# Kernel optimization log

Hardware: AMD Instinct MI355X
Metric: run time of the kernel (lower is better)

Reference implementation:

```python
import jax, jax.numpy as jnp
import numpy as np

B, T, D_MODEL, N_HEADS = 2, 2048, 2048, 16
D_HEAD = D_MODEL // N_HEADS
SCALE = 1.0 / np.sqrt(D_HEAD)


def setup_inputs() -> dict:
    key = jax.random.key(0)
    ks = jax.random.split(key, 5)
    w_std = 1.0 / np.sqrt(D_MODEL)
    x = jax.random.normal(ks[0], (B, T, D_MODEL), dtype=jnp.float32)
    W_q = jax.random.normal(ks[1], (D_MODEL, D_MODEL), dtype=jnp.float32) * w_std
    W_k = jax.random.normal(ks[2], (D_MODEL, D_MODEL), dtype=jnp.float32) * w_std
    W_v = jax.random.normal(ks[3], (D_MODEL, D_MODEL), dtype=jnp.float32) * w_std
    W_o = jax.random.normal(ks[4], (D_MODEL, D_MODEL), dtype=jnp.float32) * w_std
    return {"x": x, "W_q": W_q, "W_k": W_k, "W_v": W_v, "W_o": W_o}


def _split_heads(y):
    # [B, T, D] -> [B, H, T, d_head]
    b, t, _ = y.shape
    return y.reshape(b, t, N_HEADS, D_HEAD).transpose(0, 2, 1, 3)


def reference(x, W_q, W_k, W_v, W_o):
    # Linear layers (torch nn.Linear: y = x @ W.T)
    Q = _split_heads(x @ W_q.T)
    K = _split_heads(x @ W_k.T)
    V = _split_heads(x @ W_v.T)
    # Causal softmax attention (math-equivalent to the tiled online-softmax loop)
    scores = jnp.einsum('bhqd,bhkd->bhqk', Q, K) * SCALE
    causal_mask = jnp.tril(jnp.ones((T, T), dtype=bool))  # [T, T]
    scores = jnp.where(causal_mask, scores, -jnp.inf)
    P = jax.nn.softmax(scores, axis=-1)
    O = jnp.einsum('bhqk,bhkd->bhqd', P, V)
    out = O.transpose(0, 2, 1, 3).reshape(B, T, D_MODEL)  # merge heads
    return out @ W_o.T
```

## Files before the change

kernel.cpp:

```cpp
#include <hip/hip_runtime.h>
#include <hip/hip_bf16.h>
#include <hip/hip_fp16.h>

#define B_   2
#define T_   2048
#define DM   2048
#define NH   16
#define DH   128
#define M_   (B_*T_)
#define SCALE_ 0.08838834764831845f

typedef _Float16 f16;
typedef f16  half8 __attribute__((ext_vector_type(8)));
typedef f16  half4 __attribute__((ext_vector_type(4)));
typedef float f32x4 __attribute__((ext_vector_type(4)));

#define GL16(gp, lp) __builtin_amdgcn_global_load_lds( \
    (const __attribute__((address_space(1))) void*)(gp), \
    (__attribute__((address_space(3))) void*)(lp), 16, 0, 0)

#define MFMA16(a, b, c) __builtin_amdgcn_mfma_f32_16x16x32_f16((a), (b), (c), 0, 0, 0)

struct CvtArgs { const float* s[5]; f16* d[5]; };

__global__ __launch_bounds__(256) void convert_all(CvtArgs a) {
    size_t i4 = (size_t)blockIdx.x * 256 + threadIdx.x;
    int r; size_t off;
    if (i4 < 2097152) { r = 0; off = i4; }
    else { size_t k = i4 - 2097152; r = 1 + (int)(k >> 20); off = k & 1048575; }
    float4 v = *((const float4*)a.s[r] + off);
    half4 h;
    h[0] = (f16)v.x; h[1] = (f16)v.y; h[2] = (f16)v.z; h[3] = (f16)v.w;
    *((half4*)a.d[r] + off) = h;
}

#define NT_K 32

__global__ __launch_bounds__(256, 2)
void qkv3(const f16* __restrict__ A, const f16* __restrict__ Bw,
          f16* __restrict__ dst)
{
    __shared__ __align__(16) char smem[81920];

    const int tid  = threadIdx.x;
    const int lane = tid & 63;
    const int w    = tid >> 6;
    const int wr   = w >> 1, wc = w & 1;

    const int id = (blockIdx.x & 7) * 128 + (blockIdx.x >> 3);
    const int bm = id & 31, bn = id >> 5;
    const int m0 = bm * 128, n0 = bn * 192;

    const int scol8 = (((tid & 7) ^ ((tid >> 3) & 7)) << 3);
    const int rc0 = (((lane >> 4) * 16)      ) ^ ((lane & 7) << 4);
    const int rc1 = (64 + (lane >> 4) * 16   ) ^ ((lane & 7) << 4);

    f32x4 acc[4][6] = {};

#define QSA(bufb, s, kt) GL16( \
    A + (size_t)(m0 + (s)*32 + (tid>>3)) * 2048 + (kt)*64 + scol8, \
    smem + (bufb)*40960 + (s)*4096 + w*1024)
#define QSB(bufb, u, kt) GL16( \
    Bw + (size_t)(n0 + (u)*32 + (tid>>3)) * 2048 + (kt)*64 + scol8, \
    smem + (bufb)*40960 + 16384 + (u)*4096 + w*1024)

    QSA(0, 0, 0); QSA(0, 1, 0); QSA(0, 2, 0); QSA(0, 3, 0);
    QSB(0, 0, 0); QSB(0, 3, 0); QSB(0, 1, 0); QSB(0, 4, 0);
    QSB(0, 2, 0); QSB(0, 5, 0);

    const int abase = wr * 8192 + (lane & 15) * 128;
    const int bbase = 16384 + wc * 12288 + (lane & 15) * 128;

#define GATE(n_) do { \
    asm volatile("s_waitcnt vmcnt(" #n_ ")" ::: "memory"); \
    __builtin_amdgcn_s_barrier(); \
    __builtin_amdgcn_sched_barrier(0); \
} while (0)

#define MFC(BB, f_) do { \
    __builtin_amdgcn_s_setprio(1); \
    _Pragma("unroll") \
    for (int m_ = 0; m_ < 4; ++m_) { \
        acc[m_][f_] = MFMA16(af[m_][0], (BB)[0], acc[m_][f_]); \
        acc[m_][f_] = MFMA16(af[m_][1], (BB)[1], acc[m_][f_]); \
    } \
    __builtin_amdgcn_s_setprio(0); \
} while (0)

#define RDB(dstv, off) do { \
    const char* p_ = buf + bbase + (off); \
    dstv[0] = *(const half8*)(p_ + rc0); \
    dstv[1] = *(const half8*)(p_ + rc1); \
} while (0)

    for (int t = 0; t < NT_K; ++t) {
        const int c = t & 1;
        const char* buf = smem + c * 40960;
        const int kt = (t + 1 < NT_K) ? t + 1 : t;

        half8 af[4][2], be[2], bo[2];

        GATE(4);

        #pragma unroll
        for (int m = 0; m < 4; ++m) {
            const char* p = buf + abase + m * 2048;
            af[m][0] = *(const half8*)(p + rc0);
            af[m][1] = *(const half8*)(p + rc1);
        }
        RDB(be, 0);
        QSA(c ^ 1, 0, kt); QSA(c ^ 1, 1, kt);
        MFC(be, 0);

        RDB(bo, 2048);
        QSA(c ^ 1, 2, kt); QSA(c ^ 1, 3, kt);
        MFC(bo, 1);

        GATE(6);

        RDB(be, 4096);
        QSB(c ^ 1, 0, kt); QSB(c ^ 1, 3, kt);
        MFC(be, 2);

        RDB(bo, 6144);
        QSB(c ^ 1, 1, kt); QSB(c ^ 1, 4, kt);
        MFC(bo, 3);

        GATE(8);

        RDB(be, 8192);
        QSB(c ^ 1, 2, kt); QSB(c ^ 1, 5, kt);
        MFC(be, 4);

        RDB(bo, 10240);
        MFC(bo, 5);
    }
#undef RDB
#undef MFC
#undef GATE
#undef QSA
#undef QSB

    asm volatile("s_waitcnt vmcnt(0)" ::: "memory");

    #pragma unroll
    for (int m = 0; m < 4; ++m)
        #pragma unroll
        for (int f = 0; f < 6; ++f)
            #pragma unroll
            for (int j = 0; j < 4; ++j) {
                int row  = m0 + wr * 64 + m * 16 + (lane >> 4) * 4 + j;
                int gcol = n0 + wc * 96 + f * 16 + (lane & 15);
                int sec = gcol >> 11, cic = gcol & 2047;
                int b = row >> 11, tt = row & (T_ - 1);
                int h = cic >> 7, d = cic & 127;
                float cs = (sec == 0) ? SCALE_ : 1.0f;
                dst[(size_t)sec * ((size_t)M_ * 2048) +
                    ((size_t)(b * NH + h) * T_ + tt) * DH + d] = (f16)(acc[m][f][j] * cs);
            }
}

#define NT_W 32

__global__ __launch_bounds__(512, 4)
void wo2(const f16* __restrict__ A, const f16* __restrict__ Bw,
         float* __restrict__ Cf)
{
    __shared__ __align__(16) char smem[65536];

    const int tid  = threadIdx.x;
    const int lane = tid & 63;
    const int w    = tid >> 6;
    const int wr   = w >> 2, wc = w & 3;

    const int id = (blockIdx.x & 7) * 64 + (blockIdx.x >> 3);
    const int bm = id & 31, bn = id >> 5;
    const int m0 = bm * 128, n0 = bn * 128;

    const int scol8 = (((tid & 7) ^ ((tid >> 3) & 7)) << 3);
    const int rc0 = (((lane >> 4) * 16)      ) ^ ((lane & 7) << 4);
    const int rc1 = (64 + (lane >> 4) * 16   ) ^ ((lane & 7) << 4);

    f32x4 acc[4][2] = {};

#define WSTAGE_A(bufb, s, kt) GL16( \
    A + (size_t)(m0 + (tid>>8)*64 + (s)*32 + ((tid>>3)&31)) * 2048 + (kt)*64 + scol8, \
    smem + (bufb)*32768 + (s)*8192 + w*1024)
#define WSTAGE_B(bufb, u, kt) GL16( \
    Bw + (size_t)(n0 + (tid>>7)*32 + (u)*16 + ((tid>>3)&15)) * 2048 + (kt)*64 + scol8, \
    smem + (bufb)*32768 + 16384 + (u)*8192 + w*1024)

    WSTAGE_A(0, 0, 0); WSTAGE_A(0, 1, 0);
    WSTAGE_B(0, 0, 0); WSTAGE_B(0, 1, 0);

    const int abase = wr * 4096 + (lane & 15) * 128;
    const int bbase = 16384 + (wc * 16 + (lane & 15)) * 128;

    for (int t = 0; t < NT_W; ++t) {
        const int c  = t & 1;
        const char* buf = smem + c * 32768;
        const int kt = (t + 1 < NT_W) ? t + 1 : t;

        half8 af[4][2], bfr[2];
        asm volatile("s_waitcnt vmcnt(1)" ::: "memory");
        __builtin_amdgcn_s_barrier();
        __builtin_amdgcn_sched_barrier(0);
        #pragma unroll
        for (int m = 0; m < 4; ++m) {
            const char* p = buf + (m >> 1) * 8192 + abase + (m & 1) * 2048;
            af[m][0] = *(const half8*)(p + rc0);
            af[m][1] = *(const half8*)(p + rc1);
        }
        { const char* p = buf + bbase;
          bfr[0] = *(const half8*)(p + rc0); bfr[1] = *(const half8*)(p + rc1); }
        WSTAGE_A(c ^ 1, 0, kt); WSTAGE_A(c ^ 1, 1, kt);
        __builtin_amdgcn_s_setprio(1);
        #pragma unroll
        for (int m = 0; m < 4; ++m) {
            acc[m][0] = MFMA16(af[m][0], bfr[0], acc[m][0]);
            acc[m][0] = MFMA16(af[m][1], bfr[1], acc[m][0]);
        }
        __builtin_amdgcn_s_setprio(0);

        asm volatile("s_waitcnt vmcnt(2)" ::: "memory");
        __builtin_amdgcn_s_barrier();
        __builtin_amdgcn_sched_barrier(0);
        { const char* p = buf + bbase + 8192;
          bfr[0] = *(const half8*)(p + rc0); bfr[1] = *(const half8*)(p + rc1); }
        WSTAGE_B(c ^ 1, 0, kt); WSTAGE_B(c ^ 1, 1, kt);
        __builtin_amdgcn_s_setprio(1);
        #pragma unroll
        for (int m = 0; m < 4; ++m) {
            acc[m][1] = MFMA16(af[m][0], bfr[0], acc[m][1]);
            acc[m][1] = MFMA16(af[m][1], bfr[1], acc[m][1]);
        }
        __builtin_amdgcn_s_setprio(0);
        __builtin_amdgcn_s_barrier();
    }
#undef WSTAGE_A
#undef WSTAGE_B

    asm volatile("s_waitcnt vmcnt(0)" ::: "memory");

    #pragma unroll
    for (int m = 0; m < 4; ++m)
        #pragma unroll
        for (int u = 0; u < 2; ++u)
            #pragma unroll
            for (int j = 0; j < 4; ++j) {
                int row = m0 + wr * 64 + m * 16 + (lane >> 4) * 4 + j;
                int col = n0 + wc * 32 + u * 16 + (lane & 15);
                Cf[(size_t)row * 2048 + col] = acc[m][u][j];
            }
}

__global__ __launch_bounds__(256)
void vtrans(const f16* __restrict__ Vin, f16* __restrict__ Vout)
{
    __shared__ f16 ld[64][72];
    const int tid = threadIdx.x;
    const int dd = blockIdx.x;
    const int tt = blockIdx.y;
    const int bh = blockIdx.z;

    const int r  = tid >> 2;
    const int s2 = (tid & 3) * 2;

    const f16* src = Vin + ((size_t)bh * T_ + tt * 64 + r) * DH + dd * 64;
    half8 v0 = *(const half8*)(src + s2 * 8);
    half8 v1 = *(const half8*)(src + s2 * 8 + 8);
    #pragma unroll
    for (int e = 0; e < 8; ++e) ld[s2 * 8 + e][r]     = v0[e];
    #pragma unroll
    for (int e = 0; e < 8; ++e) ld[s2 * 8 + 8 + e][r] = v1[e];
    __syncthreads();

    f16* dst = Vout + ((size_t)bh * DH + dd * 64 + r) * T_ + tt * 64;
    *(half8*)(dst + s2 * 8)     = *(const half8*)&ld[r][s2 * 8];
    *(half8*)(dst + s2 * 8 + 8) = *(const half8*)&ld[r][s2 * 8 + 8];
}

#define QB 64
#define KB 64
#define PP 72
#define NQT (T_/QB)

__global__ __launch_bounds__(256, 4)
void attn_fwd(const f16* __restrict__ Q, const f16* __restrict__ K,
              const f16* __restrict__ Vt, f16* __restrict__ O)
{
    __shared__ __align__(16) char Ks[2][16384];
    __shared__ __align__(16) char Vs[2][16384];
    __shared__ __align__(16) f16 Ps[4][16][PP];

    const int tid  = threadIdx.x;
    const int lane = tid & 63;
    const int w    = tid >> 6;
    const int g    = lane >> 4;

    const int bid  = blockIdx.x;
    const int swz  = (bid & 7) * 64 + (bid >> 3);
    const int bh   = swz >> 4;
    const int pair = swz & 15;
    const size_t base = (size_t)bh * T_ * DH;
    const int b = bh >> 4, h = bh & 15;

    const int krow0 = w * 4 + g;
    const int kswz  = ((lane & 15) ^ (krow0 & 7)) << 3;
    const int vrow0 = w * 8 + (lane >> 3);
    const int vswz  = (((lane & 7) ^ ((lane >> 3) & 7)) << 3);

#define STAGE_K(c_, kv) do { \
    _Pragma("unroll") for (int i_ = 0; i_ < 4; ++i_) { \
        const f16* g_ = K + base + (size_t)((kv) + i_*16 + krow0) * DH + kswz; \
        GL16(g_, &Ks[c_][i_*4096 + w*1024]); } } while (0)
#define STAGE_V(c_, kv) do { \
    _Pragma("unroll") for (int i_ = 0; i_ < 4; ++i_) { \
        const f16* g_ = Vt + base + (size_t)(i_*32 + vrow0) * T_ + (kv) + vswz; \
        GL16(g_, &Vs[c_][i_*4096 + w*1024]); } } while (0)

    #pragma unroll
    for (int hf = 0; hf < 2; ++hf) {
        const int qt = (hf == 0) ? pair : (NQT - 1 - pair);
        const int q0 = qt * QB;
        const int ntiles = qt + 1;
        const int qg = q0 + w * 16 + (lane & 15);

        half8 qf[4];
        #pragma unroll
        for (int kk = 0; kk < 4; ++kk)
            qf[kk] = *reinterpret_cast<const half8*>(
                &Q[base + (size_t)qg * DH + kk * 32 + g * 8]);

        float mrun = -1e30f, lrun = 0.f;
        f32x4 o[8] = {};

        __syncthreads();
        STAGE_K(0, 0);
        STAGE_V(0, 0);

        for (int it = 0; it < ntiles; ++it) {
            const int c = it & 1;
            __syncthreads();
            if (it + 1 < ntiles) {
                STAGE_K(c ^ 1, (it + 1) * KB);
                STAGE_V(c ^ 1, (it + 1) * KB);
            }

            const char* kb = &Ks[c][0];
            f32x4 sacc[4] = {};
            __builtin_amdgcn_s_setprio(1);
            #pragma unroll
            for (int n = 0; n < 4; ++n)
                #pragma unroll
                for (int kk = 0; kk < 4; ++kk) {
                    half8 kfv = *(const half8*)(kb + (n*16 + (lane & 15)) * 256 +
                        ((kk*32 + g * 8) * 2 ^ ((lane & 7) << 4)));
                    sacc[n] = MFMA16(kfv, qf[kk], sacc[n]);
                }
            __builtin_amdgcn_s_setprio(0);

            if (it == ntiles - 1) {
                #pragma unroll
                for (int n = 0; n < 4; ++n)
                    #pragma unroll
                    for (int j = 0; j < 4; ++j) {
                        int kg = it * KB + n*16 + g*4 + j;
                        if (kg > qg) sacc[n][j] = -1e30f;
                    }
            }

            float mx = sacc[0][0];
            #pragma unroll
            for (int n = 0; n < 4; ++n)
                #pragma unroll
                for (int j = 0; j < 4; ++j) mx = fmaxf(mx, sacc[n][j]);
            mx = fmaxf(mx, __shfl_xor(mx, 16));
            mx = fmaxf(mx, __shfl_xor(mx, 32));
            float mnew = fmaxf(mrun, mx);
            float sf = __expf(mrun - mnew);
            float rs = 0.f;
            #pragma unroll
            for (int n = 0; n < 4; ++n)
                #pragma unroll
                for (int j = 0; j < 4; ++j) {
                    float p = __expf(sacc[n][j] - mnew);
                    sacc[n][j] = p;
                    rs += p;
                }
            rs += __shfl_xor(rs, 16);
            rs += __shfl_xor(rs, 32);
            lrun = lrun * sf + rs;
            mrun = mnew;
            #pragma unroll
            for (int nn = 0; nn < 8; ++nn) o[nn] *= sf;

            #pragma unroll
            for (int n = 0; n < 4; ++n) {
                half4 hv;
                hv[0] = (f16)sacc[n][0]; hv[1] = (f16)sacc[n][1];
                hv[2] = (f16)sacc[n][2]; hv[3] = (f16)sacc[n][3];
                *reinterpret_cast<half4*>(&Ps[w][lane & 15][n*16 + g*4]) = hv;
            }

            half8 bp[2];
            #pragma unroll
            for (int cc = 0; cc < 2; ++cc)
                bp[cc] = *reinterpret_cast<const half8*>(&Ps[w][lane & 15][cc*32 + g*8]);

            const char* vb = &Vs[c][0];
            __builtin_amdgcn_s_setprio(1);
            #pragma unroll
            for (int n = 0; n < 8; ++n)
                #pragma unroll
                for (int cc = 0; cc < 2; ++cc) {
                    half8 vf = *(const half8*)(vb + (n*16 + (lane & 15)) * 128 +
                        ((cc*64 + g*16) ^ ((lane & 7) << 4)));
                    o[n] = MFMA16(vf, bp[cc], o[n]);
                }
            __builtin_amdgcn_s_setprio(0);
        }

        float invl = 1.0f / lrun;
        #pragma unroll
        for (int n = 0; n < 8; ++n) {
            half4 hv;
            hv[0] = (f16)(o[n][0] * invl); hv[1] = (f16)(o[n][1] * invl);
            hv[2] = (f16)(o[n][2] * invl); hv[3] = (f16)(o[n][3] * invl);
            *reinterpret_cast<half4*>(
                &O[((size_t)(b * T_ + qg) * NH + h) * DH + n*16 + g*4]) = hv;
        }
    }
#undef STAGE_K
#undef STAGE_V
}

extern "C" void kernel_launch(void* const* d_in, const int* in_sizes, int n_in,
                              void* d_out, int out_size, void* d_ws, size_t ws_size,
                              hipStream_t stream)
{
    const float* x  = (const float*)d_in[0];
    const float* wq = (const float*)d_in[1];
    const float* wk = (const float*)d_in[2];
    const float* wv = (const float*)d_in[3];
    const float* wo = (const float*)d_in[4];
    float* out = (float*)d_out;

    const size_t nx = (size_t)M_ * DM;
    const size_t nw = (size_t)DM * DM;
    const size_t need = (nx * 5 + nw * 4) * sizeof(f16);
    if (ws_size < need) return;

    char* ws = (char*)d_ws;
    f16* xh  = (f16*)ws;  ws += nx * 2;
    f16* wqh = (f16*)ws;  ws += nw * 2;
    f16* wkh = (f16*)ws;  ws += nw * 2;
    f16* wvh = (f16*)ws;  ws += nw * 2;
    f16* woh = (f16*)ws;  ws += nw * 2;
    f16* Qh  = (f16*)ws;  ws += nx * 2;
    f16* Kh  = (f16*)ws;  ws += nx * 2;
    f16* Vh  = (f16*)ws;  ws += nx * 2;
    f16* Oh  = (f16*)ws;  ws += nx * 2;

    f16* Vth = xh;

    CvtArgs ca;
    ca.s[0] = x;  ca.d[0] = xh;
    ca.s[1] = wq; ca.d[1] = wqh;
    ca.s[2] = wk; ca.d[2] = wkh;
    ca.s[3] = wv; ca.d[3] = wvh;
    ca.s[4] = wo; ca.d[4] = woh;
    convert_all<<<24576, 256, 0, stream>>>(ca);

    qkv3<<<dim3(1024), 256, 0, stream>>>(xh, wqh, Qh);

    vtrans<<<dim3(2, 32, 32), 256, 0, stream>>>(Vh, Vth);

    attn_fwd<<<dim3(512), 256, 0, stream>>>(Qh, Kh, Vth, Oh);

    wo2<<<dim3(512), 512, 0, stream>>>(Oh, woh, out);
}
```

Measured before the change: 239.5 us.

## Enlarge QKV GEMM tile to 256x192 with 8-wave blocks and new pipeline

The fused QKV projection GEMM moves from 256-thread blocks computing 128x192 tiles to 512-thread blocks computing 256x192 tiles, halving the grid. Shared memory grows to double-buffered 56 KB stages, and the A/B staging layout and block swizzle are rearranged. The k-loop schedule is rewritten with finer barriers between prefetch issue and MFMA groups. The aim is more operand reuse per loaded B tile and fewer redundant global loads. The cost is more barriers per iteration and higher LDS use, which likely allows only one block per CU.

```diff
diff --git a/kernel.cpp b/kernel.cpp
--- a/kernel.cpp
+++ b/kernel.cpp
@@ -36,20 +36,20 @@
 
 #define NT_K 32
 
-__global__ __launch_bounds__(256, 2)
+__global__ __launch_bounds__(512, 2)
 void qkv3(const f16* __restrict__ A, const f16* __restrict__ Bw,
           f16* __restrict__ dst)
 {
-    __shared__ __align__(16) char smem[81920];
+    __shared__ __align__(16) char smem[114688];
 
     const int tid  = threadIdx.x;
     const int lane = tid & 63;
     const int w    = tid >> 6;
     const int wr   = w >> 1, wc = w & 1;
 
-    const int id = (blockIdx.x & 7) * 128 + (blockIdx.x >> 3);
-    const int bm = id & 31, bn = id >> 5;
-    const int m0 = bm * 128, n0 = bn * 192;
+    const int id = (blockIdx.x & 7) * 64 + (blockIdx.x >> 3);
+    const int bm = id & 15, bn = id >> 4;
+    const int m0 = bm * 256, n0 = bn * 192;
 
     const int scol8 = (((tid & 7) ^ ((tid >> 3) & 7)) << 3);
     const int rc0 = (((lane >> 4) * 16)      ) ^ ((lane & 7) << 4);
@@ -57,23 +57,25 @@
 
     f32x4 acc[4][6] = {};
 
-#define QSA(bufb, s, kt) GL16( \
-    A + (size_t)(m0 + (s)*32 + (tid>>3)) * 2048 + (kt)*64 + scol8, \
-    smem + (bufb)*40960 + (s)*4096 + w*1024)
-#define QSB(bufb, u, kt) GL16( \
-    Bw + (size_t)(n0 + (u)*32 + (tid>>3)) * 2048 + (kt)*64 + scol8, \
-    smem + (bufb)*40960 + 16384 + (u)*4096 + w*1024)
-
-    QSA(0, 0, 0); QSA(0, 1, 0); QSA(0, 2, 0); QSA(0, 3, 0);
-    QSB(0, 0, 0); QSB(0, 3, 0); QSB(0, 1, 0); QSB(0, 4, 0);
-    QSB(0, 2, 0); QSB(0, 5, 0);
-
-    const int abase = wr * 8192 + (lane & 15) * 128;
-    const int bbase = 16384 + wc * 12288 + (lane & 15) * 128;
-
-#define GATE(n_) do { \
-    asm volatile("s_waitcnt vmcnt(" #n_ ")" ::: "memory"); \
+#define QSTAGE_A(bufb, ch, s, kt) GL16( \
+    A + (size_t)(m0 + (ch)*128 + (tid>>8)*64 + (s)*32 + ((tid>>3)&31)) * 2048 + (kt)*64 + scol8, \
+    smem + (bufb)*57344 + (ch)*16384 + (s)*8192 + w*1024)
+#define QSTAGE_B(bufb, u, kt) GL16( \
+    Bw + (size_t)(n0 + (tid>>7)*48 + (u)*16 + ((tid>>3)&15)) * 2048 + (kt)*64 + scol8, \
+    smem + (bufb)*57344 + 32768 + (u)*8192 + w*1024)
+
+    const int abase = (wr >> 1) * 16384 + (wr & 1) * 4096 + (lane & 15) * 128;
+    const int bbase = 32768 + wc * 4096 + (lane & 15) * 128;
+
+    QSTAGE_A(0, 0, 0, 0); QSTAGE_A(0, 0, 1, 0);
+    QSTAGE_A(0, 1, 0, 0); QSTAGE_A(0, 1, 1, 0);
+    QSTAGE_B(0, 0, 0);    QSTAGE_B(0, 1, 0);    QSTAGE_B(0, 2, 0);
+    asm volatile("s_waitcnt vmcnt(2)" ::: "memory");
+    __builtin_amdgcn_s_barrier();
+
+#define BAR_I() do { \
     __builtin_amdgcn_s_barrier(); \
+    asm volatile("s_waitcnt lgkmcnt(0)" ::: "memory"); \
     __builtin_amdgcn_sched_barrier(0); \
 } while (0)
 
@@ -87,6 +89,13 @@
     __builtin_amdgcn_s_setprio(0); \
 } while (0)
 
+#define GATE_TAIL(n_) do { \
+    asm volatile("s_waitcnt vmcnt(" #n_ ")" ::: "memory"); \
+    __builtin_amdgcn_s_barrier(); \
+} while (0)
+
+#define BAR_II() __builtin_amdgcn_s_barrier()
+
 #define RDB(dstv, off) do { \
     const char* p_ = buf + bbase + (off); \
     dstv[0] = *(const half8*)(p_ + rc0); \
@@ -95,51 +104,59 @@
 
     for (int t = 0; t < NT_K; ++t) {
         const int c = t & 1;
-        const char* buf = smem + c * 40960;
+        const char* buf = smem + c * 57344;
         const int kt = (t + 1 < NT_K) ? t + 1 : t;
 
         half8 af[4][2], be[2], bo[2];
 
-        GATE(4);
-
         #pragma unroll
         for (int m = 0; m < 4; ++m) {
-            const char* p = buf + abase + m * 2048;
+            const char* p = buf + (m >> 1) * 8192 + abase + (m & 1) * 2048;
             af[m][0] = *(const half8*)(p + rc0);
             af[m][1] = *(const half8*)(p + rc1);
         }
         RDB(be, 0);
-        QSA(c ^ 1, 0, kt); QSA(c ^ 1, 1, kt);
+        QSTAGE_A(c ^ 1, 0, 0, kt); QSTAGE_A(c ^ 1, 0, 1, kt);
+        BAR_I();
         MFC(be, 0);
+        BAR_II();
 
         RDB(bo, 2048);
-        QSA(c ^ 1, 2, kt); QSA(c ^ 1, 3, kt);
-        MFC(bo, 1);
-
-        GATE(6);
-
-        RDB(be, 4096);
-        QSB(c ^ 1, 0, kt); QSB(c ^ 1, 3, kt);
+        QSTAGE_A(c ^ 1, 1, 0, kt); QSTAGE_A(c ^ 1, 1, 1, kt);
+        BAR_I();
+        MFC(bo, 3);
+        GATE_TAIL(5);
+
+        RDB(be, 8192);
+        QSTAGE_B(c ^ 1, 0, kt);
+        BAR_I();
+        MFC(be, 1);
+        BAR_II();
+
+        RDB(bo, 8192 + 2048);
+        QSTAGE_B(c ^ 1, 1, kt);
+        BAR_I();
+        MFC(bo, 4);
+        GATE_TAIL(6);
+
+        RDB(be, 16384);
+        QSTAGE_B(c ^ 1, 2, kt);
+        BAR_I();
         MFC(be, 2);
-
-        RDB(bo, 6144);
-        QSB(c ^ 1, 1, kt); QSB(c ^ 1, 4, kt);
-        MFC(bo, 3);
-
-        GATE(8);
-
-        RDB(be, 8192);
-        QSB(c ^ 1, 2, kt); QSB(c ^ 1, 5, kt);
-        MFC(be, 4);
-
-        RDB(bo, 10240);
+        BAR_II();
+
+        RDB(bo, 16384 + 2048);
+        BAR_I();
         MFC(bo, 5);
+        GATE_TAIL(2);
     }
 #undef RDB
+#undef BAR_II
+#undef GATE_TAIL
 #undef MFC
-#undef GATE
-#undef QSA
-#undef QSB
+#undef BAR_I
+#undef QSTAGE_A
+#undef QSTAGE_B
 
     asm volatile("s_waitcnt vmcnt(0)" ::: "memory");
 
@@ -472,7 +489,7 @@
     ca.s[4] = wo; ca.d[4] = woh;
     convert_all<<<24576, 256, 0, stream>>>(ca);
 
-    qkv3<<<dim3(1024), 256, 0, stream>>>(xh, wqh, Qh);
+    qkv3<<<dim3(512), 512, 0, stream>>>(xh, wqh, Qh);
 
     vtrans<<<dim3(2, 32, 32), 256, 0, stream>>>(Vh, Vth);
 
```

After: 243.8 us. No clear change (+1.8%).
